# Performance work log

Hardware: AMD Instinct MI355X
Metric: run time of the kernel (lower is better)

The kernel has to match this reference:

```python
import jax, jax.numpy as jnp
import numpy as np
import math

WP, WF = 10, 10      # past/future window
EPS = 1e-8           # torch cosine_similarity eps
CLIP = 1.0 - 1e-6    # keep arccos (and its grad) finite
MAXN = 110           # hard-coded alpha width in the module


def setup_inputs() -> dict:
    key = jax.random.key(0)
    k1, k2, k3, k4, k5, k6 = jax.random.split(key, 6)
    B, L, G, N, D = 32, 110, 512, 40, 300
    node_features = jax.random.normal(k1, (B, L, G), jnp.float32)
    knowledge = jax.random.normal(k2, (B, L, N, D), jnp.float32)
    anew = jax.random.uniform(k3, (B, L, N), jnp.float32)
    var_sem = 2.0 / (G + G)
    var_con = 2.0 / (D + D)
    weight_sem = jax.random.normal(k4, (G, G), jnp.float32) * var_sem
    weight_con = jax.random.normal(k5, (D, D), jnp.float32) * var_con
    text_len = jax.random.randint(k6, (B,), 55, L + 1, jnp.int32)
    return dict(node_features=node_features, knowledge=knowledge, anew=anew,
                weight_sem=weight_sem, weight_con=weight_con, text_len=text_len)


def reference(node_features, knowledge, anew, weight_sem, weight_con, text_len):
    B, L, G = node_features.shape
    N = knowledge.shape[2]
    dt = node_features.dtype

    # window + validity mask, replaces per-(i,j) python slicing: [B, j, k]
    j = jnp.arange(L)[:, None]
    k = jnp.arange(L)[None, :]
    cur = text_len[:, None, None]
    mask = (k >= j - WP) & (k <= j + WF)
    mask = mask[None] & (k[None, :, :] <= cur - 1) & (j[None, :, :] < cur)
    fmask = mask.astype(dt)

    # ---- semantic branch: score = 1 - acos(cos_sim(f_j, W_sem f_k))/pi, windowed softmax
    att_sem = jnp.einsum('st,blt->bls', weight_sem, node_features)      # [B,L,G]
    num = jnp.einsum('bjg,bkg->bjk', node_features, att_sem)
    nf = jnp.maximum(jnp.linalg.norm(node_features, axis=-1), EPS)      # [B,L]
    na = jnp.maximum(jnp.linalg.norm(att_sem, axis=-1), EPS)            # [B,L]
    cos = num / (nf[:, :, None] * na[:, None, :])
    score = 1.0 - jnp.arccos(jnp.clip(cos, -CLIP, CLIP)) / math.pi
    neg = jnp.finfo(dt).min
    s = jnp.where(mask, score, neg)
    s = s - jnp.max(s, axis=-1, keepdims=True)
    e = jnp.exp(s) * fmask
    alphas_sem = e / jnp.maximum(jnp.sum(e, axis=-1, keepdims=True), EPS)  # [B,L,L]

    # ---- affinity transform of anew: v -> (||[v, v/2] - [0.5, 0]|| - 0.06467)/0.607468
    anew_aff = (jnp.sqrt((anew - 0.5) ** 2 + (0.5 * anew) ** 2) - 0.06467) / 0.607468

    # ---- contextual branch: windowed sum_n |cos_sim(aff_feat_{k,n}, knowledge_{j,n})|
    att_con = jnp.einsum('blns,st->blnt', knowledge, weight_con)        # [B,L,N,D]
    aff_feat = att_con * anew_aff[..., None]                            # [B,L,N,D]
    num_c = jnp.einsum('bknd,bjnd->bjkn', aff_feat, knowledge)          # [B,j,k,N]
    n_f = jnp.maximum(jnp.linalg.norm(aff_feat, axis=-1), EPS)          # [B,k,N]
    n_k = jnp.maximum(jnp.linalg.norm(knowledge, axis=-1), EPS)         # [B,j,N]
    cos_c = num_c / (n_f[:, None, :, :] * n_k[:, :, None, :])
    alphas_con = 10.0 * jnp.sum(jnp.abs(cos_c), axis=-1) * fmask        # [B,j,k]

    out = 0.5 * alphas_sem + 0.5 * alphas_con                           # [B,L,L]
    if L < MAXN:  # module hard-codes width 110
        out = jnp.pad(out, ((0, 0), (0, 0), (0, MAXN - L)))
    return out
```

## Files before the change

### kernel.cpp

```cpp
#include <hip/hip_runtime.h>
#include <hip/hip_bf16.h>
#include <math.h>

constexpr int Bb   = 32;
constexpr int Ls   = 110;
constexpr int Gs   = 512;
constexpr int Ns   = 40;
constexpr int Ds   = 300;
constexpr int WPc  = 10;
constexpr int WFc  = 10;
constexpr int MAXNc = 110;
constexpr float EPSf  = 1e-8f;
constexpr float CLIPf = 1.0f - 1e-6f;
constexpr int BL = Bb * Ls;
constexpr int Mrows = BL * Ns;
constexpr int BPITCH = 328;
constexpr int KST = 320;
constexpr int RGRP = Mrows / 256;

typedef __attribute__((ext_vector_type(8))) short short8_t;
typedef __attribute__((ext_vector_type(4))) short short4_t;
typedef __attribute__((ext_vector_type(4))) float floatx4;

__device__ __forceinline__ unsigned short bf16r(float f) {
  unsigned u = __float_as_uint(f);
  u += 0x7fffu + ((u >> 16) & 1u);
  return (unsigned short)(u >> 16);
}

__device__ __forceinline__ unsigned pkbf(float lo, float hi) {
  unsigned a = __float_as_uint(lo), b = __float_as_uint(hi);
  a += 0x7fffu + ((a >> 16) & 1u);
  b += 0x7fffu + ((b >> 16) & 1u);
  return (a >> 16) | (b & 0xffff0000u);
}

__device__ __forceinline__ short8_t cvt8(const float4 v0, const float4 v1) {
  union { short8_t s; unsigned u[4]; } p;
  p.u[0] = pkbf(v0.x, v0.y);
  p.u[1] = pkbf(v0.z, v0.w);
  p.u[2] = pkbf(v1.x, v1.y);
  p.u[3] = pkbf(v1.z, v1.w);
  return p.s;
}

__global__ __launch_bounds__(256) void transpose_wsem(const float* __restrict__ w,
                                                      float* __restrict__ wt) {
  __shared__ float tile[32][33];
  const int bx = blockIdx.x * 32;
  const int by = blockIdx.y * 32;
  const int tx = threadIdx.x;
  const int ty = threadIdx.y;
#pragma unroll
  for (int r = ty; r < 32; r += 8)
    tile[r][tx] = w[(by + r) * Gs + (bx + tx)];
  __syncthreads();
#pragma unroll
  for (int r = ty; r < 32; r += 8)
    wt[(bx + r) * Gs + (by + tx)] = tile[tx][r];
}

__global__ __launch_bounds__(256) void wct_prep(const float* __restrict__ wc,
                                                short* __restrict__ wct) {
  __shared__ float tile[32][33];
  const int t0 = blockIdx.x * 32;
  const int s0 = blockIdx.y * 32;
  const int tx = threadIdx.x, ty = threadIdx.y;
#pragma unroll
  for (int r = ty; r < 32; r += 8) {
    const int s = s0 + r, t = t0 + tx;
    tile[r][tx] = (s < Ds && t < Ds) ? wc[s * Ds + t] : 0.f;
  }
  __syncthreads();
#pragma unroll
  for (int r = ty; r < 32; r += 8) {
    const int t = t0 + r, s = s0 + tx;
    wct[t * KST + s] = (short)bf16r(tile[tx][r]);
  }
}

__global__ __launch_bounds__(512) void sem_gemm(const float* __restrict__ nf,
                                                const float* __restrict__ wt,
                                                float* __restrict__ att_sem,
                                                float* __restrict__ na_arr) {
  const int bl0 = blockIdx.x * 8;
  const int s = threadIdx.x;
  const float* __restrict__ x0 = nf + (size_t)bl0 * Gs;
  float acc[8];
#pragma unroll
  for (int r = 0; r < 8; ++r) acc[r] = 0.f;
#pragma unroll 4
  for (int t = 0; t < Gs; ++t) {
    const float wv = wt[t * Gs + s];
#pragma unroll
    for (int r = 0; r < 8; ++r) acc[r] = fmaf(wv, x0[r * Gs + t], acc[r]);
  }
#pragma unroll
  for (int r = 0; r < 8; ++r) att_sem[(size_t)(bl0 + r) * Gs + s] = acc[r];

  __shared__ float partial[8][8];
  const int wave = s >> 6, lane = s & 63;
#pragma unroll
  for (int r = 0; r < 8; ++r) {
    float v = acc[r] * acc[r];
#pragma unroll
    for (int off = 32; off > 0; off >>= 1) v += __shfl_xor(v, off);
    if (lane == 0) partial[r][wave] = v;
  }
  __syncthreads();
  if (s < 8) {
    float sum = 0.f;
#pragma unroll
    for (int w2 = 0; w2 < 8; ++w2) sum += partial[s][w2];
    na_arr[bl0 + s] = fmaxf(sqrtf(sum), EPSf);
  }
}

__global__ __launch_bounds__(256) void sem_attn(const float* __restrict__ nf,
                                                const float* __restrict__ att_sem,
                                                const float* __restrict__ na_arr,
                                                const int* __restrict__ tlen,
                                                float* __restrict__ out) {
  const int blk = blockIdx.x;
  const int b = blk / Ls, j = blk % Ls;
  const int len = tlen[b];
  float* __restrict__ orow = out + (size_t)(b * Ls + j) * MAXNc;
  if (j >= len) {
    for (int k = threadIdx.x; k < MAXNc; k += 256) orow[k] = 0.f;
    return;
  }
  const int k0 = max(j - WPc, 0);
  const int k1 = min(j + WFc, len - 1);
  const int nk = k1 - k0 + 1;

  __shared__ float xs[Gs];
  __shared__ float sc[21];
  __shared__ float red[4];

  const float* __restrict__ x = nf + (size_t)(b * Ls + j) * Gs;
  float ss = 0.f;
  for (int t = threadIdx.x; t < Gs; t += 256) {
    const float v = x[t];
    xs[t] = v;
    ss += v * v;
  }
  const int wave = threadIdx.x >> 6, lane = threadIdx.x & 63;
#pragma unroll
  for (int off = 32; off > 0; off >>= 1) ss += __shfl_xor(ss, off);
  if (lane == 0) red[wave] = ss;
  __syncthreads();
  const float nfn = fmaxf(sqrtf(red[0] + red[1] + red[2] + red[3]), EPSf);

  for (int i = wave; i < nk; i += 4) {
    const int k = k0 + i;
    const float* __restrict__ as = att_sem + (size_t)(b * Ls + k) * Gs;
    float d = 0.f;
#pragma unroll
    for (int t = lane; t < Gs; t += 64) d = fmaf(xs[t], as[t], d);
#pragma unroll
    for (int off = 32; off > 0; off >>= 1) d += __shfl_xor(d, off);
    if (lane == 0) {
      float cs = d / (nfn * na_arr[b * Ls + k]);
      cs = fminf(fmaxf(cs, -CLIPf), CLIPf);
      sc[i] = 1.0f - acosf(cs) * (float)(1.0 / M_PI);
    }
  }
  __syncthreads();
  if (threadIdx.x == 0) {
    float m = -1e30f;
    for (int i = 0; i < nk; ++i) m = fmaxf(m, sc[i]);
    red[0] = m;
  }
  __syncthreads();
  const float m = red[0];
  if ((int)threadIdx.x < nk) sc[threadIdx.x] = expf(sc[threadIdx.x] - m);
  __syncthreads();
  if (threadIdx.x == 0) {
    float s = 0.f;
    for (int i = 0; i < nk; ++i) s += sc[i];
    red[1] = 1.0f / fmaxf(s, EPSf);
  }
  __syncthreads();
  const float inv = red[1];
  for (int k = threadIdx.x; k < MAXNc; k += 256) {
    float v = 0.f;
    if (k >= k0 && k <= k1) v = 0.5f * sc[k - k0] * inv;
    orow[k] = v;
  }
}

__global__ __launch_bounds__(256, 2) void con_gemm_mfma(const float* __restrict__ kn,
                                                        const short* __restrict__ wct,
                                                        const int* __restrict__ tlen,
                                                        unsigned short* __restrict__ ybar,
                                                        float* __restrict__ rowss) {
  const int lin = blockIdx.x;
  const int xcd = lin & 7, slot = lin >> 3;
  const int m = slot & 3;
  const int g = xcd + 8 * (slot >> 2);
  if (g >= RGRP) return;
  const int rowbase = g * 256;
  const int n0 = m * 80;

  __shared__ short Bl[80 * BPITCH];
  const int tid = threadIdx.x;
  for (int s = tid; s < 80 * 40; s += 256) {
    const int nl = s / 40, sl = s % 40;
    *reinterpret_cast<short8_t*>(&Bl[nl * BPITCH + sl * 8]) =
        *reinterpret_cast<const short8_t*>(wct + (n0 + nl) * KST + sl * 8);
  }
  __syncthreads();

  const int wave = tid >> 6, lane = tid & 63;
  const int quad = lane >> 4, l16 = lane & 15;
  const int wrow = rowbase + wave * 64;

  {
    bool any = false;
    for (int bl = wrow / Ns; bl <= (wrow + 63) / Ns; ++bl)
      any |= (bl % Ls) < tlen[bl / Ls];
    if (!any) return;
  }

  const float* arow[4];
#pragma unroll
  for (int tt = 0; tt < 4; ++tt)
    arow[tt] = kn + (size_t)(wrow + tt * 16 + l16) * Ds + quad * 8;

  floatx4 acc[4][5];
#pragma unroll
  for (int tt = 0; tt < 4; ++tt)
#pragma unroll
    for (int i = 0; i < 5; ++i) acc[tt][i] = (floatx4){0.f, 0.f, 0.f, 0.f};

  float4 F0[4], F1[4];
#pragma unroll
  for (int tt = 0; tt < 4; ++tt) {
    F0[tt] = *reinterpret_cast<const float4*>(arow[tt]);
    F1[tt] = *reinterpret_cast<const float4*>(arow[tt] + 4);
  }

#pragma unroll
  for (int c = 0; c < 10; ++c) {
    short8_t Af[4];
#pragma unroll
    for (int tt = 0; tt < 4; ++tt) Af[tt] = cvt8(F0[tt], F1[tt]);
    if (c < 8) {
#pragma unroll
      for (int tt = 0; tt < 4; ++tt) {
        F0[tt] = *reinterpret_cast<const float4*>(arow[tt] + (c + 1) * 32);
        F1[tt] = *reinterpret_cast<const float4*>(arow[tt] + (c + 1) * 32 + 4);
      }
    } else if (c == 8) {
#pragma unroll
      for (int tt = 0; tt < 4; ++tt) {
        float4 v0 = make_float4(0.f, 0.f, 0.f, 0.f);
        float4 v1 = make_float4(0.f, 0.f, 0.f, 0.f);
        if (quad == 0) {
          v0 = *reinterpret_cast<const float4*>(arow[tt] + 288);
          v1 = *reinterpret_cast<const float4*>(arow[tt] + 292);
        } else if (quad == 1) {
          v0 = *reinterpret_cast<const float4*>(arow[tt] + 288);
        }
        F0[tt] = v0;
        F1[tt] = v1;
      }
    }
#pragma unroll
    for (int i = 0; i < 5; ++i) {
      const short8_t bfrag = *reinterpret_cast<const short8_t*>(
          &Bl[(i * 16 + l16) * BPITCH + c * 32 + quad * 8]);
#pragma unroll
      for (int tt = 0; tt < 4; ++tt)
        acc[tt][i] = __builtin_amdgcn_mfma_f32_16x16x32_bf16(Af[tt], bfrag,
                                                             acc[tt][i], 0, 0, 0);
    }
  }

#pragma unroll
  for (int tt = 0; tt < 4; ++tt) {
    const int row0 = wrow + tt * 16;
    const int blA = row0 / Ns, blB = (row0 + 15) / Ns;
    const bool alive = ((blA % Ls) < tlen[blA / Ls]) | ((blB % Ls) < tlen[blB / Ls]);
    if (!alive) continue;

#pragma unroll
    for (int r = 0; r < 4; ++r) {
      float p = 0.f;
#pragma unroll
      for (int i = 0; i < 5; ++i) p = fmaf(acc[tt][i][r], acc[tt][i][r], p);
      p += __shfl_xor(p, 1);
      p += __shfl_xor(p, 2);
      p += __shfl_xor(p, 4);
      p += __shfl_xor(p, 8);
      if (l16 == 0) atomicAdd(&rowss[row0 + quad * 4 + r], p);
    }
#pragma unroll
    for (int i = 0; i < 5; ++i) {
      const int col = n0 + i * 16 + l16;
#pragma unroll
      for (int r = 0; r < 4; ++r)
        ybar[(size_t)(row0 + quad * 4 + r) * KST + col] = bf16r(acc[tt][i][r]);
    }
  }
}

__global__ __launch_bounds__(512) void con_attn_mfma(const float* __restrict__ kn,
                                                     const unsigned short* __restrict__ ybar,
                                                     const float* __restrict__ rowss,
                                                     const float* __restrict__ anew,
                                                     const int* __restrict__ tlen,
                                                     float* __restrict__ out) {
  const int lin = blockIdx.x;
  const int xcd = lin & 7, slot = lin >> 3;
  const int b = xcd * 4 + slot / 7;
  const int jt = slot % 7;
  const int j0 = jt * 16;
  const int len = tlen[b];
  if (j0 >= len) return;
  const int kbase = min(max(j0 - WPc, 0), Ls - 48);

  const int tid = threadIdx.x;
  const int wave = tid >> 6, lane = tid & 63;
  const int quad = lane >> 4, l16 = lane & 15;

  __shared__ float red[8][768];

  const int jj = min(j0 + l16, Ls - 1);
  const size_t blj = (size_t)(b * Ls + jj);

  float outacc[3][4];
#pragma unroll
  for (int t = 0; t < 3; ++t)
#pragma unroll
    for (int r = 0; r < 4; ++r) outacc[t][r] = 0.f;

  const unsigned short* yrow[3];
  int krow_m[3];
#pragma unroll
  for (int t = 0; t < 3; ++t) {
    const int k = kbase + t * 16 + l16;
    yrow[t] = ybar + (size_t)(b * Ls + k) * Ns * KST;
    krow_m[t] = (b * Ls + k) * Ns;
  }

  for (int ni = 0; ni < 5; ++ni) {
    const int n = wave + ni * 8;
    const float* __restrict__ arow = kn + (blj * Ns + n) * (size_t)Ds + quad * 8;

    float w_t[3];
#pragma unroll
    for (int t = 0; t < 3; ++t) {
      const int mm = krow_m[t] + n;
      const float a = anew[mm];
      const float ssqk = rowss[mm];
      const float aff = (sqrtf((a - 0.5f) * (a - 0.5f) + 0.25f * a * a) - 0.06467f) *
                        (1.0f / 0.607468f);
      w_t[t] = aff / fmaxf(aff * sqrtf(ssqk), EPSf);
    }

    floatx4 S[3];
#pragma unroll
    for (int t = 0; t < 3; ++t) S[t] = (floatx4){0.f, 0.f, 0.f, 0.f};
    float ssq = 0.f;

#pragma unroll
    for (int c = 0; c < 10; ++c) {
      float4 v0 = make_float4(0.f, 0.f, 0.f, 0.f);
      float4 v1 = make_float4(0.f, 0.f, 0.f, 0.f);
      if (c < 9) {
        v0 = *reinterpret_cast<const float4*>(arow + c * 32);
        v1 = *reinterpret_cast<const float4*>(arow + c * 32 + 4);
      } else {
        if (quad == 0) {
          v0 = *reinterpret_cast<const float4*>(arow + 288);
          v1 = *reinterpret_cast<const float4*>(arow + 292);
        } else if (quad == 1) {
          v0 = *reinterpret_cast<const float4*>(arow + 288);
        }
      }
      ssq += v0.x * v0.x + v0.y * v0.y + v0.z * v0.z + v0.w * v0.w +
             v1.x * v1.x + v1.y * v1.y + v1.z * v1.z + v1.w * v1.w;
      const short8_t afrag = cvt8(v0, v1);
#pragma unroll
      for (int t = 0; t < 3; ++t) {
        const short8_t bfrag = *reinterpret_cast<const short8_t*>(
            yrow[t] + (size_t)n * KST + c * 32 + quad * 8);
        S[t] = __builtin_amdgcn_mfma_f32_16x16x32_bf16(afrag, bfrag, S[t], 0, 0, 0);
      }
    }

    ssq += __shfl_xor(ssq, 16);
    ssq += __shfl_xor(ssq, 32);
    const float kinv = 1.0f / fmaxf(sqrtf(ssq), EPSf);

#pragma unroll
    for (int r = 0; r < 4; ++r) {
      const float kv = __shfl(kinv, quad * 4 + r);
#pragma unroll
      for (int t = 0; t < 3; ++t)
        outacc[t][r] = fmaf(kv * w_t[t], fabsf(S[t][r]), outacc[t][r]);
    }
  }

#pragma unroll
  for (int t = 0; t < 3; ++t)
#pragma unroll
    for (int r = 0; r < 4; ++r)
      red[wave][(quad * 4 + r) * 48 + t * 16 + l16] = outacc[t][r];
  __syncthreads();

  for (int idx = tid; idx < 768; idx += 512) {
    float s = 0.f;
#pragma unroll
    for (int w = 0; w < 8; ++w) s += red[w][idx];
    const int j = j0 + idx / 48;
    const int k = kbase + idx % 48;
    if (j < len && k < len && k >= j - WPc && k <= j + WFc)
      out[(size_t)(b * Ls + j) * MAXNc + k] += 5.0f * s;
  }
}

extern "C" void kernel_launch(void* const* d_in, const int* in_sizes, int n_in,
                              void* d_out, int out_size, void* d_ws, size_t ws_size,
                              hipStream_t stream) {
  const float* nf   = (const float*)d_in[0];
  const float* kn   = (const float*)d_in[1];
  const float* anew = (const float*)d_in[2];
  const float* wsem = (const float*)d_in[3];
  const float* wcon = (const float*)d_in[4];
  const int*   tlen = (const int*)d_in[5];
  float* out = (float*)d_out;

  float* att_sem = (float*)d_ws;
  float* na_arr  = att_sem + (size_t)BL * Gs;
  float* wt      = na_arr + BL;
  short* wct     = (short*)(wt + (size_t)Gs * Gs);
  float* rowss   = (float*)(wct + KST * KST);
  unsigned short* ybar = (unsigned short*)(rowss + Mrows);

  hipMemsetAsync(rowss, 0, (size_t)Mrows * sizeof(float), stream);
  transpose_wsem<<<dim3(16, 16), dim3(32, 8), 0, stream>>>(wsem, wt);
  wct_prep<<<dim3(10, 10), dim3(32, 8), 0, stream>>>(wcon, wct);
  sem_gemm<<<BL / 8, 512, 0, stream>>>(nf, wt, att_sem, na_arr);
  sem_attn<<<BL, 256, 0, stream>>>(nf, att_sem, na_arr, tlen, out);
  con_gemm_mfma<<<2208, 256, 0, stream>>>(kn, wct, tlen, ybar, rowss);
  con_attn_mfma<<<Bb * 7, 512, 0, stream>>>(kn, ybar, rowss, anew, tlen, out);
}
```

Measured before the change: 503.7 us.

## Pre-swizzle W_con into MFMA fragment layout and drop LDS staging in con GEMM

W_con is now pre-packed into per-lane bf16 MFMA B-fragment order, so each wave loads its B fragments directly from global/L2 with coalesced 16-byte loads. This replaces the shared-memory tile and its __syncthreads. Each wave now handles 32 rows instead of 64, the grid doubles, and launch bounds allow 4 blocks per CU for more occupancy. The trade-off is less reuse of B per load, since each fragment now feeds 2 MFMAs instead of 4, and B traffic from cache goes up.

Result: slower. 516.7 us (+2.6%).

```diff
diff --git a/kernel.cpp b/kernel.cpp
--- a/kernel.cpp
+++ b/kernel.cpp
@@ -14,9 +14,8 @@
 constexpr float CLIPf = 1.0f - 1e-6f;
 constexpr int BL = Bb * Ls;
 constexpr int Mrows = BL * Ns;
-constexpr int BPITCH = 328;
 constexpr int KST = 320;
-constexpr int RGRP = Mrows / 256;
+constexpr int RG2 = Mrows / 128;
 
 typedef __attribute__((ext_vector_type(8))) short short8_t;
 typedef __attribute__((ext_vector_type(4))) short short4_t;
@@ -60,23 +59,21 @@
     wt[(bx + r) * Gs + (by + tx)] = tile[tx][r];
 }
 
-__global__ __launch_bounds__(256) void wct_prep(const float* __restrict__ wc,
-                                                short* __restrict__ wct) {
-  __shared__ float tile[32][33];
-  const int t0 = blockIdx.x * 32;
-  const int s0 = blockIdx.y * 32;
-  const int tx = threadIdx.x, ty = threadIdx.y;
-#pragma unroll
-  for (int r = ty; r < 32; r += 8) {
-    const int s = s0 + r, t = t0 + tx;
-    tile[r][tx] = (s < Ds && t < Ds) ? wc[s * Ds + t] : 0.f;
-  }
-  __syncthreads();
-#pragma unroll
-  for (int r = ty; r < 32; r += 8) {
-    const int t = t0 + r, s = s0 + tx;
-    wct[t * KST + s] = (short)bf16r(tile[tx][r]);
-  }
+__global__ __launch_bounds__(64) void wctf_prep(const float* __restrict__ wc,
+                                                short* __restrict__ wctf) {
+  const int fid = blockIdx.x;
+  const int nb = fid / 10, c = fid % 10;
+  const int lane = threadIdx.x;
+  const int t = nb * 16 + (lane & 15);
+  const int s0 = c * 32 + (lane >> 4) * 8;
+  short8_t v;
+#pragma unroll
+  for (int e = 0; e < 8; ++e) {
+    const int s = s0 + e;
+    const float f = (s < Ds && t < Ds) ? wc[s * Ds + t] : 0.f;
+    v[e] = (short)bf16r(f);
+  }
+  *reinterpret_cast<short8_t*>(wctf + ((size_t)fid * 64 + lane) * 8) = v;
 }
 
 __global__ __launch_bounds__(512) void sem_gemm(const float* __restrict__ nf,
@@ -189,8 +186,8 @@
   }
 }
 
-__global__ __launch_bounds__(256, 2) void con_gemm_mfma(const float* __restrict__ kn,
-                                                        const short* __restrict__ wct,
+__global__ __launch_bounds__(256, 4) void con_gemm_mfma(const float* __restrict__ kn,
+                                                        const short* __restrict__ wctf,
                                                         const int* __restrict__ tlen,
                                                         unsigned short* __restrict__ ybar,
                                                         float* __restrict__ rowss) {
@@ -198,62 +195,60 @@
   const int xcd = lin & 7, slot = lin >> 3;
   const int m = slot & 3;
   const int g = xcd + 8 * (slot >> 2);
-  if (g >= RGRP) return;
-  const int rowbase = g * 256;
-  const int n0 = m * 80;
-
-  __shared__ short Bl[80 * BPITCH];
+  if (g >= RG2) return;
+
   const int tid = threadIdx.x;
-  for (int s = tid; s < 80 * 40; s += 256) {
-    const int nl = s / 40, sl = s % 40;
-    *reinterpret_cast<short8_t*>(&Bl[nl * BPITCH + sl * 8]) =
-        *reinterpret_cast<const short8_t*>(wct + (n0 + nl) * KST + sl * 8);
-  }
-  __syncthreads();
-
   const int wave = tid >> 6, lane = tid & 63;
   const int quad = lane >> 4, l16 = lane & 15;
-  const int wrow = rowbase + wave * 64;
+  const int wrow = g * 128 + wave * 32;
 
   {
     bool any = false;
-    for (int bl = wrow / Ns; bl <= (wrow + 63) / Ns; ++bl)
+    for (int bl = wrow / Ns; bl <= (wrow + 31) / Ns; ++bl)
       any |= (bl % Ls) < tlen[bl / Ls];
     if (!any) return;
   }
 
-  const float* arow[4];
-#pragma unroll
-  for (int tt = 0; tt < 4; ++tt)
+  const int nb0 = m * 5;
+  const short* __restrict__ bbase = wctf + (size_t)nb0 * 5120;
+
+  const float* arow[2];
+#pragma unroll
+  for (int tt = 0; tt < 2; ++tt)
     arow[tt] = kn + (size_t)(wrow + tt * 16 + l16) * Ds + quad * 8;
 
-  floatx4 acc[4][5];
-#pragma unroll
-  for (int tt = 0; tt < 4; ++tt)
+  floatx4 acc[2][5];
+#pragma unroll
+  for (int tt = 0; tt < 2; ++tt)
 #pragma unroll
     for (int i = 0; i < 5; ++i) acc[tt][i] = (floatx4){0.f, 0.f, 0.f, 0.f};
 
-  float4 F0[4], F1[4];
-#pragma unroll
-  for (int tt = 0; tt < 4; ++tt) {
+  float4 F0[2], F1[2];
+#pragma unroll
+  for (int tt = 0; tt < 2; ++tt) {
     F0[tt] = *reinterpret_cast<const float4*>(arow[tt]);
     F1[tt] = *reinterpret_cast<const float4*>(arow[tt] + 4);
   }
 
 #pragma unroll
   for (int c = 0; c < 10; ++c) {
-    short8_t Af[4];
-#pragma unroll
-    for (int tt = 0; tt < 4; ++tt) Af[tt] = cvt8(F0[tt], F1[tt]);
+    short8_t bfr[5];
+#pragma unroll
+    for (int i = 0; i < 5; ++i)
+      bfr[i] = *reinterpret_cast<const short8_t*>(
+          bbase + ((size_t)(i * 10 + c) * 64 + lane) * 8);
+    short8_t Af[2];
+#pragma unroll
+    for (int tt = 0; tt < 2; ++tt) Af[tt] = cvt8(F0[tt], F1[tt]);
     if (c < 8) {
 #pragma unroll
-      for (int tt = 0; tt < 4; ++tt) {
+      for (int tt = 0; tt < 2; ++tt) {
         F0[tt] = *reinterpret_cast<const float4*>(arow[tt] + (c + 1) * 32);
         F1[tt] = *reinterpret_cast<const float4*>(arow[tt] + (c + 1) * 32 + 4);
       }
     } else if (c == 8) {
 #pragma unroll
-      for (int tt = 0; tt < 4; ++tt) {
+      for (int tt = 0; tt < 2; ++tt) {
         float4 v0 = make_float4(0.f, 0.f, 0.f, 0.f);
         float4 v1 = make_float4(0.f, 0.f, 0.f, 0.f);
         if (quad == 0) {
@@ -267,18 +262,16 @@
       }
     }
 #pragma unroll
-    for (int i = 0; i < 5; ++i) {
-      const short8_t bfrag = *reinterpret_cast<const short8_t*>(
-          &Bl[(i * 16 + l16) * BPITCH + c * 32 + quad * 8]);
-#pragma unroll
-      for (int tt = 0; tt < 4; ++tt)
-        acc[tt][i] = __builtin_amdgcn_mfma_f32_16x16x32_bf16(Af[tt], bfrag,
+    for (int i = 0; i < 5; ++i)
+#pragma unroll
+      for (int tt = 0; tt < 2; ++tt)
+        acc[tt][i] = __builtin_amdgcn_mfma_f32_16x16x32_bf16(Af[tt], bfr[i],
                                                              acc[tt][i], 0, 0, 0);
-    }
-  }
-
-#pragma unroll
-  for (int tt = 0; tt < 4; ++tt) {
+  }
+
+  const int n0 = m * 80;
+#pragma unroll
+  for (int tt = 0; tt < 2; ++tt) {
     const int row0 = wrow + tt * 16;
     const int blA = row0 / Ns, blB = (row0 + 15) / Ns;
     const bool alive = ((blA % Ls) < tlen[blA / Ls]) | ((blB % Ls) < tlen[blB / Ls]);
@@ -435,15 +428,15 @@
   float* att_sem = (float*)d_ws;
   float* na_arr  = att_sem + (size_t)BL * Gs;
   float* wt      = na_arr + BL;
-  short* wct     = (short*)(wt + (size_t)Gs * Gs);
-  float* rowss   = (float*)(wct + KST * KST);
+  short* wctf    = (short*)(wt + (size_t)Gs * Gs);
+  float* rowss   = (float*)(wctf + 200 * 64 * 8);
   unsigned short* ybar = (unsigned short*)(rowss + Mrows);
 
   hipMemsetAsync(rowss, 0, (size_t)Mrows * sizeof(float), stream);
   transpose_wsem<<<dim3(16, 16), dim3(32, 8), 0, stream>>>(wsem, wt);
-  wct_prep<<<dim3(10, 10), dim3(32, 8), 0, stream>>>(wcon, wct);
+  wctf_prep<<<200, 64, 0, stream>>>(wcon, wctf);
   sem_gemm<<<BL / 8, 512, 0, stream>>>(nf, wt, att_sem, na_arr);
   sem_attn<<<BL, 256, 0, stream>>>(nf, att_sem, na_arr, tlen, out);
-  con_gemm_mfma<<<2208, 256, 0, stream>>>(kn, wct, tlen, ybar, rowss);
+  con_gemm_mfma<<<4416, 256, 0, stream>>>(kn, wctf, tlen, ybar, rowss);
   con_attn_mfma<<<Bb * 7, 512, 0, stream>>>(kn, ybar, rowss, anew, tlen, out);
 }
```
